# Kernel tuning notes

Hardware: AMD Instinct MI355X
Metric: run time of the kernel (lower is better)

The kernel has to match this reference:

```python
import jax, jax.numpy as jnp
import numpy as np

B, T, D, H, C = 128, 1024, 3, 512, 3


def setup_inputs() -> dict:
    key = jax.random.key(0)
    ks = jax.random.split(key, 9)
    s = 1.0 / np.sqrt(H)
    u = lambda k, shp: jax.random.uniform(k, shp, jnp.float32, -s, s)
    return {
        'inputs': jax.random.normal(ks[0], (B, T, D), jnp.float32),
        'W': u(ks[1], (H, H)),
        'P': u(ks[2], (H, D)),
        'b_v': u(ks[3], (H, 1)),
        'W_z': u(ks[4], (H, H)),
        'P_z': u(ks[5], (H, D)),
        'b_z': u(ks[6], (H, 1)),
        'fc_W': u(ks[7], (C, H)),
        'fc_b': u(ks[8], (C,)),
    }


def reference(inputs, W, P, b_v, W_z, P_z, b_z, fc_W, fc_b):
    # Mask: second half of hidden units receive no direct input (rows H//2: of P zeroed)
    h = P.shape[0]
    P_m = jnp.concatenate([P[: h // 2], jnp.zeros_like(P[h // 2 :])], axis=0)
    bv = b_v[:, 0]
    bz = b_z[:, 0]

    def step(r, x_t):  # r: (B,H), x_t: (B,D)
        z = jax.nn.sigmoid(r @ W_z.T + x_t @ P_z.T + bz)
        cand = jax.nn.sigmoid(r @ W.T + x_t @ P_m.T + bv)
        r_new = (1.0 - z) * r + z * cand
        return r_new, r_new

    r0 = jnp.zeros((inputs.shape[0], h), inputs.dtype)
    xs = jnp.transpose(inputs, (1, 0, 2))  # (T,B,D)
    _, hs = jax.lax.scan(step, r0, xs)      # (T,B,H)
    hidden = jnp.transpose(hs, (1, 0, 2))   # (B,T,H)
    out = hidden @ fc_W.T + fc_b            # (B,T,C)
    return out, hidden
```

## Files before the change

kernel.cpp:

```cpp
#include <hip/hip_runtime.h>
#include <hip/hip_bf16.h>

#define BB 128
#define TT 1024
#define DD 3
#define HH 512
#define CC 3

#define NG 8
#define NCH 16
#define MB 16
#define HC 32

typedef __attribute__((ext_vector_type(8))) __bf16 bf16x8;
typedef __attribute__((ext_vector_type(4))) float f32x4;

__global__ __launch_bounds__(256, 1) void rnn_persist(
    const float* __restrict__ x,
    const float* __restrict__ W,
    const float* __restrict__ P,
    const float* __restrict__ bv,
    const float* __restrict__ Wz,
    const float* __restrict__ Pz,
    const float* __restrict__ bz,
    float* __restrict__ hidden,
    unsigned* __restrict__ Rbuf,
    unsigned* __restrict__ tag)
{
    __shared__ __align__(16) __bf16 Wl[64][520];
    __shared__ __align__(16) __bf16 Ra[16][520];
    __shared__ float pre[16][68];

    const int tid = threadIdx.x;
    const int bid = blockIdx.x;
    const int g   = bid & 7;
    const int ch  = bid >> 3;
    const int h0  = ch * HC;
    const int b0  = g * MB;

    for (int idx = tid; idx < 64 * 512; idx += 256) {
        int row = idx >> 9, col = idx & 511;
        float v = (row < 32) ? Wz[(h0 + row) * HH + col]
                             : W[(h0 + row - 32) * HH + col];
        Wl[row][col] = (__bf16)v;
    }

    const int lane = tid & 63;
    const int wv   = tid >> 6;
    const int frow = lane & 15;
    const int q    = lane >> 4;
    const int eb   = tid >> 4;
    const int ehp  = tid & 15;

    const int hl0 = 2 * ehp, hl1 = hl0 + 1;
    const int hg0 = h0 + hl0, hg1 = h0 + hl1;
    const float pzw00 = Pz[hg0*3+0], pzw01 = Pz[hg0*3+1], pzw02 = Pz[hg0*3+2];
    const float pzw10 = Pz[hg1*3+0], pzw11 = Pz[hg1*3+1], pzw12 = Pz[hg1*3+2];
    const float pvw00 = (hg0 < HH/2) ? P[hg0*3+0] : 0.f;
    const float pvw01 = (hg0 < HH/2) ? P[hg0*3+1] : 0.f;
    const float pvw02 = (hg0 < HH/2) ? P[hg0*3+2] : 0.f;
    const float pvw10 = (hg1 < HH/2) ? P[hg1*3+0] : 0.f;
    const float pvw11 = (hg1 < HH/2) ? P[hg1*3+1] : 0.f;
    const float pvw12 = (hg1 < HH/2) ? P[hg1*3+2] : 0.f;
    const float bzr0 = bz[hg0], bzr1 = bz[hg1];
    const float bvr0 = bv[hg0], bvr1 = bv[hg1];

    {
        unsigned* dst0 = Rbuf + (size_t)(b0 + eb) * (HH / 2) + ch * 16 + ehp;
        __hip_atomic_store(dst0, 0u, __ATOMIC_RELAXED, __HIP_MEMORY_SCOPE_AGENT);
    }
    __syncthreads();
    if (tid == 0)
        __hip_atomic_store(&tag[g * 16 + ch], 1u, __ATOMIC_RELAXED, __HIP_MEMORY_SCOPE_AGENT);

    bf16x8 Bfrag[16];
    #pragma unroll
    for (int ks = 0; ks < 16; ks++)
        Bfrag[ks] = *(const bf16x8*)&Wl[wv * 16 + frow][ks * 32 + q * 8];

    float rs0 = 0.f, rs1 = 0.f;
    const float* xptr = x + (size_t)(b0 + eb) * TT * DD;

    for (int t = 0; t < TT; t++) {
        float x0 = xptr[0], x1 = xptr[1], x2 = xptr[2];
        xptr += DD;

        if (tid < 64) {
            unsigned want = (unsigned)(t + 1);
            const unsigned* tp = tag + g * 16 + (tid & 15);
            while (true) {
                unsigned v = (tid < 16)
                    ? __hip_atomic_load(tp, __ATOMIC_RELAXED, __HIP_MEMORY_SCOPE_AGENT)
                    : 0xFFFFFFFFu;
                if (__all((int)(v >= want))) break;
            }
        }
        __syncthreads();

        {
            const uint4* p0 = (const uint4*)(Rbuf + (size_t)(t & 1) * BB * (HH / 2)
                                             + (size_t)b0 * (HH / 2)) + tid;
            const uint4* p1 = p0 + 256;
            const uint4* p2 = p0 + 512;
            const uint4* p3 = p0 + 768;
            uint4 A0, A1, A2, A3;
            asm volatile(
                "global_load_dwordx4 %0, %4, off sc0 sc1\n\t"
                "global_load_dwordx4 %1, %5, off sc0 sc1\n\t"
                "global_load_dwordx4 %2, %6, off sc0 sc1\n\t"
                "global_load_dwordx4 %3, %7, off sc0 sc1\n\t"
                "s_waitcnt vmcnt(0)"
                : "=&v"(A0), "=&v"(A1), "=&v"(A2), "=&v"(A3)
                : "v"(p0), "v"(p1), "v"(p2), "v"(p3)
                : "memory");
            char* rb = (char*)&Ra[0][0];
            const int co = (tid & 63) * 16;
            *(uint4*)(rb + (wv     ) * 1040 + co) = A0;
            *(uint4*)(rb + (wv +  4) * 1040 + co) = A1;
            *(uint4*)(rb + (wv +  8) * 1040 + co) = A2;
            *(uint4*)(rb + (wv + 12) * 1040 + co) = A3;
        }
        __syncthreads();

        f32x4 acc = {0.f, 0.f, 0.f, 0.f};
        #pragma unroll
        for (int ks = 0; ks < 16; ks++) {
            bf16x8 af = *(const bf16x8*)&Ra[frow][ks * 32 + q * 8];
            acc = __builtin_amdgcn_mfma_f32_16x16x32_bf16(af, Bfrag[ks], acc, 0, 0, 0);
        }
        #pragma unroll
        for (int r = 0; r < 4; r++)
            pre[q * 4 + r][wv * 16 + frow] = acc[r];
        __syncthreads();

        float pz0 = pre[eb][hl0]      + x0*pzw00 + x1*pzw01 + x2*pzw02 + bzr0;
        float pz1 = pre[eb][hl1]      + x0*pzw10 + x1*pzw11 + x2*pzw12 + bzr1;
        float pv0 = pre[eb][32 + hl0] + x0*pvw00 + x1*pvw01 + x2*pvw02 + bvr0;
        float pv1 = pre[eb][32 + hl1] + x0*pvw10 + x1*pvw11 + x2*pvw12 + bvr1;
        float z0 = 1.f / (1.f + __expf(-pz0));
        float z1 = 1.f / (1.f + __expf(-pz1));
        float c0 = 1.f / (1.f + __expf(-pv0));
        float c1 = 1.f / (1.f + __expf(-pv1));
        rs0 = (1.f - z0) * rs0 + z0 * c0;
        rs1 = (1.f - z1) * rs1 + z1 * c1;

        union { __bf16 h[2]; unsigned u; } pk;
        pk.h[0] = (__bf16)rs0; pk.h[1] = (__bf16)rs1;
        unsigned* dst = Rbuf + (size_t)((t + 1) & 1) * BB * (HH / 2)
                        + (size_t)(b0 + eb) * (HH / 2) + ch * 16 + ehp;
        __hip_atomic_store(dst, pk.u, __ATOMIC_RELAXED, __HIP_MEMORY_SCOPE_AGENT);
        float2 hv; hv.x = rs0; hv.y = rs1;
        *(float2*)&hidden[((size_t)(b0 + eb) * TT + t) * HH + h0 + hl0] = hv;

        __syncthreads();
        if (tid == 0)
            __hip_atomic_store(&tag[g * 16 + ch], (unsigned)(t + 2),
                               __ATOMIC_RELAXED, __HIP_MEMORY_SCOPE_AGENT);
    }
}

__global__ __launch_bounds__(256) void fc_kernel(
    const float* __restrict__ hidden, const float* __restrict__ fcW,
    const float* __restrict__ fcb, float* __restrict__ out)
{
    const int lane = threadIdx.x & 63;
    const int wid  = (blockIdx.x * blockDim.x + threadIdx.x) >> 6;
    const int nw   = (gridDim.x * blockDim.x) >> 6;
    const int NR   = BB * TT;

    float w0[8], w1[8], w2[8];
    #pragma unroll
    for (int j = 0; j < 8; j++) {
        w0[j] = fcW[0 * HH + lane * 8 + j];
        w1[j] = fcW[1 * HH + lane * 8 + j];
        w2[j] = fcW[2 * HH + lane * 8 + j];
    }
    const float c0 = fcb[0], c1 = fcb[1], c2 = fcb[2];

    int row = wid;
    float4 va, vb;
    if (row < NR) {
        const float* hr = hidden + (size_t)row * HH + lane * 8;
        va = *(const float4*)hr;
        vb = *(const float4*)(hr + 4);
    }
    while (row < NR) {
        int nrow = row + nw;
        float4 na, nb;
        if (nrow < NR) {
            const float* hr = hidden + (size_t)nrow * HH + lane * 8;
            na = *(const float4*)hr;
            nb = *(const float4*)(hr + 4);
        }
        float s0 = va.x*w0[0] + va.y*w0[1] + va.z*w0[2] + va.w*w0[3]
                 + vb.x*w0[4] + vb.y*w0[5] + vb.z*w0[6] + vb.w*w0[7];
        float s1 = va.x*w1[0] + va.y*w1[1] + va.z*w1[2] + va.w*w1[3]
                 + vb.x*w1[4] + vb.y*w1[5] + vb.z*w1[6] + vb.w*w1[7];
        float s2 = va.x*w2[0] + va.y*w2[1] + va.z*w2[2] + va.w*w2[3]
                 + vb.x*w2[4] + vb.y*w2[5] + vb.z*w2[6] + vb.w*w2[7];
        #pragma unroll
        for (int off = 1; off < 64; off <<= 1) {
            s0 += __shfl_xor(s0, off);
            s1 += __shfl_xor(s1, off);
            s2 += __shfl_xor(s2, off);
        }
        if (lane == 0) {
            float* o = out + (size_t)row * CC;
            o[0] = s0 + c0; o[1] = s1 + c1; o[2] = s2 + c2;
        }
        row = nrow; va = na; vb = nb;
    }
}

extern "C" void kernel_launch(void* const* d_in, const int* in_sizes, int n_in,
                              void* d_out, int out_size, void* d_ws, size_t ws_size,
                              hipStream_t stream) {
    (void)in_sizes; (void)n_in; (void)out_size; (void)ws_size;
    const float* x   = (const float*)d_in[0];
    const float* W   = (const float*)d_in[1];
    const float* P   = (const float*)d_in[2];
    const float* bv  = (const float*)d_in[3];
    const float* Wz  = (const float*)d_in[4];
    const float* Pz  = (const float*)d_in[5];
    const float* bz  = (const float*)d_in[6];
    const float* fcW = (const float*)d_in[7];
    const float* fcb = (const float*)d_in[8];

    float* out    = (float*)d_out;
    float* hidden = out + (size_t)BB * TT * CC;

    unsigned* tag  = (unsigned*)d_ws;
    unsigned* Rbuf = (unsigned*)((char*)d_ws + 4096);

    hipMemsetAsync(d_ws, 0, 4096, stream);
    hipLaunchKernelGGL(rnn_persist, dim3(NG * NCH), dim3(256), 0, stream,
                       x, W, P, bv, Wz, Pz, bz, hidden, Rbuf, tag);
    hipLaunchKernelGGL(fc_kernel, dim3(1024), dim3(256), 0, stream,
                       hidden, fcW, fcb, out);
}
```

Before: 2.342 ms.

## Replace per-step tag barrier with data-embedded step tags in recurrent state

Each 32-bit word of the shared recurrent state buffer now carries a bf16 hidden value in the upper half and the timestep in the lower half. Consumers poll the data itself until all tags match, so the separate tag flag, its wait loop and the extra block barriers per step are removed. Step zero skips the matmul because the state is zero, and a one-time ready handshake replaces the initial tag. The cost is that each step loads twice as many bytes of state, and the bounded spin can fall through on stale data if a producer is very late.

```diff
diff --git a/kernel.cpp b/kernel.cpp
--- a/kernel.cpp
+++ b/kernel.cpp
@@ -25,7 +25,7 @@
     const float* __restrict__ bz,
     float* __restrict__ hidden,
     unsigned* __restrict__ Rbuf,
-    unsigned* __restrict__ tag)
+    unsigned* __restrict__ ready)
 {
     __shared__ __align__(16) __bf16 Wl[64][520];
     __shared__ __align__(16) __bf16 Ra[16][520];
@@ -66,12 +66,25 @@
     const float bvr0 = bv[hg0], bvr1 = bv[hg1];
 
     {
-        unsigned* dst0 = Rbuf + (size_t)(b0 + eb) * (HH / 2) + ch * 16 + ehp;
-        __hip_atomic_store(dst0, 0u, __ATOMIC_RELAXED, __HIP_MEMORY_SCOPE_AGENT);
+        uint2 cl; cl.x = 0xFFFFFFFFu; cl.y = 0xFFFFFFFFu;
+        unsigned* d0 = Rbuf + (size_t)(b0 + eb) * HH + h0 + hl0;
+        unsigned* d1 = d0 + BB * HH;
+        asm volatile("global_store_dwordx2 %0, %2, off sc0 sc1\n\t"
+                     "global_store_dwordx2 %1, %2, off sc0 sc1\n\t"
+                     "s_waitcnt vmcnt(0)"
+                     :: "v"(d0), "v"(d1), "v"(cl) : "memory");
     }
     __syncthreads();
     if (tid == 0)
-        __hip_atomic_store(&tag[g * 16 + ch], 1u, __ATOMIC_RELAXED, __HIP_MEMORY_SCOPE_AGENT);
+        __hip_atomic_store(&ready[bid], 1u, __ATOMIC_RELAXED, __HIP_MEMORY_SCOPE_AGENT);
+    if (tid < 16) {
+        const unsigned* rp = &ready[tid * 8 + g];
+        int spin = 0;
+        while (__hip_atomic_load(rp, __ATOMIC_RELAXED, __HIP_MEMORY_SCOPE_AGENT) == 0u) {
+            if (++spin > (1 << 20)) break;
+        }
+    }
+    __syncthreads();
 
     bf16x8 Bfrag[16];
     #pragma unroll
@@ -81,62 +94,91 @@
     float rs0 = 0.f, rs1 = 0.f;
     const float* xptr = x + (size_t)(b0 + eb) * TT * DD;
 
+    const int c4 = tid & 127;
+    const int r0 = tid >> 7;
+    char* rb = (char*)&Ra[0][0] + r0 * 1040 + c4 * 8;
+
+    #define BAD4(G) ((((G).x ^ w16) | ((G).y ^ w16) | ((G).z ^ w16) | ((G).w ^ w16)) & 0xFFFFu)
+
     for (int t = 0; t < TT; t++) {
         float x0 = xptr[0], x1 = xptr[1], x2 = xptr[2];
         xptr += DD;
 
-        if (tid < 64) {
-            unsigned want = (unsigned)(t + 1);
-            const unsigned* tp = tag + g * 16 + (tid & 15);
-            while (true) {
-                unsigned v = (tid < 16)
-                    ? __hip_atomic_load(tp, __ATOMIC_RELAXED, __HIP_MEMORY_SCOPE_AGENT)
-                    : 0xFFFFFFFFu;
-                if (__all((int)(v >= want))) break;
+        float mz0, mz1, mc0, mc1;
+        if (t > 0) {
+            const unsigned w16 = (unsigned)t;
+            const unsigned* bse = Rbuf + (size_t)(t & 1) * (BB * HH)
+                                + (size_t)(b0 + r0) * HH + (c4 << 2);
+            const uint4* q0 = (const uint4*)(bse);
+            const uint4* q1 = (const uint4*)(bse + 1024);
+            const uint4* q2 = (const uint4*)(bse + 2048);
+            const uint4* q3 = (const uint4*)(bse + 3072);
+            const uint4* q4 = (const uint4*)(bse + 4096);
+            const uint4* q5 = (const uint4*)(bse + 5120);
+            const uint4* q6 = (const uint4*)(bse + 6144);
+            const uint4* q7 = (const uint4*)(bse + 7168);
+            uint4 G0, G1, G2, G3, G4, G5, G6, G7;
+            int spin = 0;
+            for (;;) {
+                asm volatile(
+                    "global_load_dwordx4 %0, %8, off sc0 sc1\n\t"
+                    "global_load_dwordx4 %1, %9, off sc0 sc1\n\t"
+                    "global_load_dwordx4 %2, %10, off sc0 sc1\n\t"
+                    "global_load_dwordx4 %3, %11, off sc0 sc1\n\t"
+                    "global_load_dwordx4 %4, %12, off sc0 sc1\n\t"
+                    "global_load_dwordx4 %5, %13, off sc0 sc1\n\t"
+                    "global_load_dwordx4 %6, %14, off sc0 sc1\n\t"
+                    "global_load_dwordx4 %7, %15, off sc0 sc1\n\t"
+                    "s_waitcnt vmcnt(0)"
+                    : "=&v"(G0), "=&v"(G1), "=&v"(G2), "=&v"(G3),
+                      "=&v"(G4), "=&v"(G5), "=&v"(G6), "=&v"(G7)
+                    : "v"(q0), "v"(q1), "v"(q2), "v"(q3),
+                      "v"(q4), "v"(q5), "v"(q6), "v"(q7)
+                    : "memory");
+                unsigned bad = BAD4(G0) | BAD4(G1) | BAD4(G2) | BAD4(G3)
+                             | BAD4(G4) | BAD4(G5) | BAD4(G6) | BAD4(G7);
+                if (bad == 0u) break;
+                if (++spin > (1 << 12)) break;
             }
-        }
-        __syncthreads();
-
-        {
-            const uint4* p0 = (const uint4*)(Rbuf + (size_t)(t & 1) * BB * (HH / 2)
-                                             + (size_t)b0 * (HH / 2)) + tid;
-            const uint4* p1 = p0 + 256;
-            const uint4* p2 = p0 + 512;
-            const uint4* p3 = p0 + 768;
-            uint4 A0, A1, A2, A3;
-            asm volatile(
-                "global_load_dwordx4 %0, %4, off sc0 sc1\n\t"
-                "global_load_dwordx4 %1, %5, off sc0 sc1\n\t"
-                "global_load_dwordx4 %2, %6, off sc0 sc1\n\t"
-                "global_load_dwordx4 %3, %7, off sc0 sc1\n\t"
-                "s_waitcnt vmcnt(0)"
-                : "=&v"(A0), "=&v"(A1), "=&v"(A2), "=&v"(A3)
-                : "v"(p0), "v"(p1), "v"(p2), "v"(p3)
-                : "memory");
-            char* rb = (char*)&Ra[0][0];
-            const int co = (tid & 63) * 16;
-            *(uint4*)(rb + (wv     ) * 1040 + co) = A0;
-            *(uint4*)(rb + (wv +  4) * 1040 + co) = A1;
-            *(uint4*)(rb + (wv +  8) * 1040 + co) = A2;
-            *(uint4*)(rb + (wv + 12) * 1040 + co) = A3;
-        }
-        __syncthreads();
-
-        f32x4 acc = {0.f, 0.f, 0.f, 0.f};
-        #pragma unroll
-        for (int ks = 0; ks < 16; ks++) {
-            bf16x8 af = *(const bf16x8*)&Ra[frow][ks * 32 + q * 8];
-            acc = __builtin_amdgcn_mfma_f32_16x16x32_bf16(af, Bfrag[ks], acc, 0, 0, 0);
-        }
-        #pragma unroll
-        for (int r = 0; r < 4; r++)
-            pre[q * 4 + r][wv * 16 + frow] = acc[r];
-        __syncthreads();
-
-        float pz0 = pre[eb][hl0]      + x0*pzw00 + x1*pzw01 + x2*pzw02 + bzr0;
-        float pz1 = pre[eb][hl1]      + x0*pzw10 + x1*pzw11 + x2*pzw12 + bzr1;
-        float pv0 = pre[eb][32 + hl0] + x0*pvw00 + x1*pvw01 + x2*pvw02 + bvr0;
-        float pv1 = pre[eb][32 + hl1] + x0*pvw10 + x1*pvw11 + x2*pvw12 + bvr1;
+            { uint2 o; o.x=(G0.x>>16)|(G0.y&0xFFFF0000u); o.y=(G0.z>>16)|(G0.w&0xFFFF0000u);
+              *(uint2*)(rb + 0*2080) = o; }
+            { uint2 o; o.x=(G1.x>>16)|(G1.y&0xFFFF0000u); o.y=(G1.z>>16)|(G1.w&0xFFFF0000u);
+              *(uint2*)(rb + 1*2080) = o; }
+            { uint2 o; o.x=(G2.x>>16)|(G2.y&0xFFFF0000u); o.y=(G2.z>>16)|(G2.w&0xFFFF0000u);
+              *(uint2*)(rb + 2*2080) = o; }
+            { uint2 o; o.x=(G3.x>>16)|(G3.y&0xFFFF0000u); o.y=(G3.z>>16)|(G3.w&0xFFFF0000u);
+              *(uint2*)(rb + 3*2080) = o; }
+            { uint2 o; o.x=(G4.x>>16)|(G4.y&0xFFFF0000u); o.y=(G4.z>>16)|(G4.w&0xFFFF0000u);
+              *(uint2*)(rb + 4*2080) = o; }
+            { uint2 o; o.x=(G5.x>>16)|(G5.y&0xFFFF0000u); o.y=(G5.z>>16)|(G5.w&0xFFFF0000u);
+              *(uint2*)(rb + 5*2080) = o; }
+            { uint2 o; o.x=(G6.x>>16)|(G6.y&0xFFFF0000u); o.y=(G6.z>>16)|(G6.w&0xFFFF0000u);
+              *(uint2*)(rb + 6*2080) = o; }
+            { uint2 o; o.x=(G7.x>>16)|(G7.y&0xFFFF0000u); o.y=(G7.z>>16)|(G7.w&0xFFFF0000u);
+              *(uint2*)(rb + 7*2080) = o; }
+            __syncthreads();
+
+            f32x4 acc = {0.f, 0.f, 0.f, 0.f};
+            #pragma unroll
+            for (int ks = 0; ks < 16; ks++) {
+                bf16x8 af = *(const bf16x8*)&Ra[frow][ks * 32 + q * 8];
+                acc = __builtin_amdgcn_mfma_f32_16x16x32_bf16(af, Bfrag[ks], acc, 0, 0, 0);
+            }
+            #pragma unroll
+            for (int r = 0; r < 4; r++)
+                pre[q * 4 + r][wv * 16 + frow] = acc[r];
+            __syncthreads();
+
+            mz0 = pre[eb][hl0];      mz1 = pre[eb][hl1];
+            mc0 = pre[eb][32 + hl0]; mc1 = pre[eb][32 + hl1];
+        } else {
+            mz0 = mz1 = mc0 = mc1 = 0.f;
+        }
+
+        float pz0 = mz0 + x0*pzw00 + x1*pzw01 + x2*pzw02 + bzr0;
+        float pz1 = mz1 + x0*pzw10 + x1*pzw11 + x2*pzw12 + bzr1;
+        float pv0 = mc0 + x0*pvw00 + x1*pvw01 + x2*pvw02 + bvr0;
+        float pv1 = mc1 + x0*pvw10 + x1*pvw11 + x2*pvw12 + bvr1;
         float z0 = 1.f / (1.f + __expf(-pz0));
         float z1 = 1.f / (1.f + __expf(-pz1));
         float c0 = 1.f / (1.f + __expf(-pv0));
@@ -144,19 +186,24 @@
         rs0 = (1.f - z0) * rs0 + z0 * c0;
         rs1 = (1.f - z1) * rs1 + z1 * c1;
 
-        union { __bf16 h[2]; unsigned u; } pk;
-        pk.h[0] = (__bf16)rs0; pk.h[1] = (__bf16)rs1;
-        unsigned* dst = Rbuf + (size_t)((t + 1) & 1) * BB * (HH / 2)
-                        + (size_t)(b0 + eb) * (HH / 2) + ch * 16 + ehp;
-        __hip_atomic_store(dst, pk.u, __ATOMIC_RELAXED, __HIP_MEMORY_SCOPE_AGENT);
-        float2 hv; hv.x = rs0; hv.y = rs1;
-        *(float2*)&hidden[((size_t)(b0 + eb) * TT + t) * HH + h0 + hl0] = hv;
-
-        __syncthreads();
-        if (tid == 0)
-            __hip_atomic_store(&tag[g * 16 + ch], (unsigned)(t + 2),
-                               __ATOMIC_RELAXED, __HIP_MEMORY_SCOPE_AGENT);
-    }
+        if (t < TT - 1) {
+            unsigned tagv = (unsigned)(t + 1);
+            union { __bf16 h; unsigned short u; } a0, a1;
+            a0.h = (__bf16)rs0; a1.h = (__bf16)rs1;
+            uint2 d; d.x = ((unsigned)a0.u << 16) | tagv;
+                     d.y = ((unsigned)a1.u << 16) | tagv;
+            unsigned* dst = Rbuf + (size_t)((t + 1) & 1) * (BB * HH)
+                          + (size_t)(b0 + eb) * HH + h0 + hl0;
+            asm volatile("global_store_dwordx2 %0, %1, off sc0 sc1"
+                         :: "v"(dst), "v"(d) : "memory");
+        }
+        union { float f[2]; uint2 u2; } hvu;
+        hvu.f[0] = rs0; hvu.f[1] = rs1;
+        float* hid = &hidden[((size_t)(b0 + eb) * TT + t) * HH + h0 + hl0];
+        asm volatile("global_store_dwordx2 %0, %1, off"
+                     :: "v"(hid), "v"(hvu.u2) : "memory");
+    }
+    #undef BAD4
 }
 
 __global__ __launch_bounds__(256) void fc_kernel(
@@ -229,12 +276,12 @@
     float* out    = (float*)d_out;
     float* hidden = out + (size_t)BB * TT * CC;
 
-    unsigned* tag  = (unsigned*)d_ws;
-    unsigned* Rbuf = (unsigned*)((char*)d_ws + 4096);
+    unsigned* ready = (unsigned*)d_ws;
+    unsigned* Rbuf  = (unsigned*)((char*)d_ws + 4096);
 
     hipMemsetAsync(d_ws, 0, 4096, stream);
     hipLaunchKernelGGL(rnn_persist, dim3(NG * NCH), dim3(256), 0, stream,
-                       x, W, P, bv, Wz, Pz, bz, hidden, Rbuf, tag);
+                       x, W, P, bv, Wz, Pz, bz, hidden, Rbuf, ready);
     hipLaunchKernelGGL(fc_kernel, dim3(1024), dim3(256), 0, stream,
                        hidden, fcW, fcb, out);
 }
```

Result: slower. 2.421 ms (+3.4%).
